# Kernel optimization log

Hardware: AMD Instinct MI355X
Metric: run time of the kernel (lower is better)

The kernel has to match this reference:

```python
import jax, jax.numpy as jnp
import numpy as np

KS = 3
STRIDE = 2
ALPHA = 16


def _parabolic_kernel(t, ks=KS, alpha=ALPHA):
    # z_i = linspace(-ks//2 + 1, ks//2, ks)  (python floor-div semantics)
    lo = (-ks) // 2 + 1
    hi = ks // 2
    z_i = jnp.linspace(float(lo), float(hi), ks, dtype=jnp.float32)
    z_c = z_i[:, None] ** 2 + z_i[None, :] ** 2            # [ks, ks]
    # per-channel structuring function h: [C, ks, ks]
    return -(z_c[None, :, :] / t[:, None, None]) ** alpha


def setup_inputs() -> dict:
    key = jax.random.key(0)
    kf, kt = jax.random.split(key)
    B, C, H, W = 16, 128, 224, 224
    f = jax.random.normal(kf, (B, C, H, W), dtype=jnp.float32)
    # init='uniform' -> U(0, 4); keep away from 0 to avoid fp32 overflow of (z/t)^16
    t = 0.5 + 3.5 * jax.random.uniform(kt, (C,), dtype=jnp.float32)
    return {"f": f, "t": t}


def reference(f, t):
    # Morphological dilation-style pooling: out = max over window of (f + h)
    h = _parabolic_kernel(t)                               # [C, ks, ks]
    B, C, H, W = f.shape
    Ho = (H - KS) // STRIDE + 1
    Wo = (W - KS) // STRIDE + 1
    out = jnp.full((B, C, Ho, Wo), -jnp.inf, dtype=f.dtype)
    for ki in range(KS):            # fixed 3x3 kernel: small static loop
        for kj in range(KS):
            win = f[:, :, ki:ki + (Ho - 1) * STRIDE + 1:STRIDE,
                          kj:kj + (Wo - 1) * STRIDE + 1:STRIDE]  # [B,C,Ho,Wo]
            out = jnp.maximum(out, win + h[None, :, ki, kj, None, None])
    return out
```

## Files before the change

### kernel.cpp

```cpp
#include <hip/hip_runtime.h>
#include <math.h>


namespace {
constexpr int Bn = 16, Cn = 128, Hn = 224, Wn = 224;
constexpr int Ho = 111, Wo = 111;
constexpr int ROWS_PER_BLOCK = 8;
}

__global__ __launch_bounds__(256) void lfp_kernel(const float* __restrict__ f,
                                                  const float* __restrict__ t,
                                                  float* __restrict__ out) {
    const int j  = threadIdx.x;
    const int bc = blockIdx.z;
    const int c  = bc & (Cn - 1);

    const float tc = t[c];
    const float xe = 1.0f / tc, xc = 2.0f / tc;
    float e2 = xe * xe, e4 = e2 * e2, e8 = e4 * e4;
    float c2 = xc * xc, c4 = c2 * c2, c8 = c4 * c4;
    const float hE = -(e8 * e8);
    const float hC = -(c8 * c8);

    if (j >= 56) return;
    const int col  = 4 * j;
    const int ecol = (col + 4 < Wn) ? col + 4 : Wn - 1;

    const float* fplane = f + (size_t)bc * Hn * Wn;
    float* oplane = out + (size_t)bc * Ho * Wo;

#pragma unroll
    for (int ii = 0; ii < 2; ++ii) {
        const int i = blockIdx.y * ROWS_PER_BLOCK + ii * 4 + threadIdx.y;
        if (i < Ho) {
            const float* base = fplane + (size_t)(2 * i) * Wn;
            float me = -INFINITY, mo = -INFINITY;
#pragma unroll
            for (int ki = 0; ki < 3; ++ki) {
                const float4 v = *(const float4*)(base + (size_t)ki * Wn + col);
                const float  e = base[(size_t)ki * Wn + ecol];
                const float hA = (ki == 1) ? hE : hC;
                const float hB = (ki == 1) ? 0.0f : hE;
                me = fmaxf(me, fmaxf(fmaxf(v.x + hA, v.y + hB), v.z + hA));
                mo = fmaxf(mo, fmaxf(fmaxf(v.z + hA, v.w + hB), e + hA));
            }
            float* orow = oplane + (size_t)i * Wo;
            orow[2 * j] = me;
            if (2 * j + 1 < Wo) orow[2 * j + 1] = mo;
        }
    }
}

extern "C" void kernel_launch(void* const* d_in, const int* in_sizes, int n_in,
                              void* d_out, int out_size, void* d_ws, size_t ws_size,
                              hipStream_t stream) {
    const float* f = (const float*)d_in[0];
    const float* t = (const float*)d_in[1];
    float* out = (float*)d_out;

    dim3 block(64, 4, 1);
    dim3 grid(1, (Ho + ROWS_PER_BLOCK - 1) / ROWS_PER_BLOCK, Bn * Cn);
    lfp_kernel<<<grid, block, 0, stream>>>(f, t, out);
}
```

Before: 560.1 us.

## Stream rows per thread with vertical reuse of shared boundary row and flat grid

Each thread now covers one column group and walks 37 consecutive output rows. The bottom input row of one output row is carried in registers and reused as the top row of the next, which cuts global loads per output from three rows to two. The 2D grid with idle lanes (56 of 64 active) becomes a dense 1D grid of exactly 3*planes*56 threads, and output writes use nontemporal stores. The trade-off is far fewer threads with a long serial loop per thread, which may lower memory-level parallelism and occupancy.

```diff
diff --git a/kernel.cpp b/kernel.cpp
--- a/kernel.cpp
+++ b/kernel.cpp
@@ -5,15 +5,20 @@
 namespace {
 constexpr int Bn = 16, Cn = 128, Hn = 224, Wn = 224;
 constexpr int Ho = 111, Wo = 111;
-constexpr int ROWS_PER_BLOCK = 8;
+constexpr int TILE = 37;
+constexpr int CT = 56;
+constexpr int PLANES = Bn * Cn;
 }
 
 __global__ __launch_bounds__(256) void lfp_kernel(const float* __restrict__ f,
                                                   const float* __restrict__ t,
                                                   float* __restrict__ out) {
-    const int j  = threadIdx.x;
-    const int bc = blockIdx.z;
-    const int c  = bc & (Cn - 1);
+    const int tid  = blockIdx.x * 256 + threadIdx.x;
+    const int flat = tid % (PLANES * CT);
+    const int rt   = tid / (PLANES * CT);
+    const int bc   = flat / CT;
+    const int jt   = flat % CT;
+    const int c    = bc & (Cn - 1);
 
     const float tc = t[c];
     const float xe = 1.0f / tc, xc = 2.0f / tc;
@@ -22,32 +27,45 @@
     const float hE = -(e8 * e8);
     const float hC = -(c8 * c8);
 
-    if (j >= 56) return;
-    const int col  = 4 * j;
+    const int col  = 4 * jt;
     const int ecol = (col + 4 < Wn) ? col + 4 : Wn - 1;
+    const bool oddValid = (2 * jt + 1) < Wo;
 
-    const float* fplane = f + (size_t)bc * Hn * Wn;
-    float* oplane = out + (size_t)bc * Ho * Wo;
+    const float* plane  = f + (size_t)bc * Hn * Wn;
+    float*       oplane = out + (size_t)bc * Ho * Wo;
 
-#pragma unroll
-    for (int ii = 0; ii < 2; ++ii) {
-        const int i = blockIdx.y * ROWS_PER_BLOCK + ii * 4 + threadIdx.y;
-        if (i < Ho) {
-            const float* base = fplane + (size_t)(2 * i) * Wn;
-            float me = -INFINITY, mo = -INFINITY;
-#pragma unroll
-            for (int ki = 0; ki < 3; ++ki) {
-                const float4 v = *(const float4*)(base + (size_t)ki * Wn + col);
-                const float  e = base[(size_t)ki * Wn + ecol];
-                const float hA = (ki == 1) ? hE : hC;
-                const float hB = (ki == 1) ? 0.0f : hE;
-                me = fmaxf(me, fmaxf(fmaxf(v.x + hA, v.y + hB), v.z + hA));
-                mo = fmaxf(mo, fmaxf(fmaxf(v.z + hA, v.w + hB), e + hA));
-            }
-            float* orow = oplane + (size_t)i * Wo;
-            orow[2 * j] = me;
-            if (2 * j + 1 < Wo) orow[2 * j + 1] = mo;
-        }
+    const int i0 = rt * TILE;
+
+    {
+    }
+    const float* r0 = plane + (size_t)(2 * i0) * Wn;
+    float4 v0 = *(const float4*)(r0 + col);
+    float  t0 = r0[ecol];
+    float prevOuterA = fmaxf(fmaxf(v0.x + hC, v0.y + hE), v0.z + hC);
+    float prevOuterB = fmaxf(fmaxf(v0.z + hC, v0.w + hE), t0 + hC);
+
+    for (int ii = 0; ii < TILE; ++ii) {
+        const int i = i0 + ii;
+        const float* rm = plane + (size_t)(2 * i + 1) * Wn;
+        const float* rb = plane + (size_t)(2 * i + 2) * Wn;
+        float4 vm = *(const float4*)(rm + col);
+        float  em = rm[ecol];
+        float4 vb = *(const float4*)(rb + col);
+        float  eb = rb[ecol];
+
+        float midA = fmaxf(fmaxf(vm.x + hE, vm.y), vm.z + hE);
+        float midB = fmaxf(fmaxf(vm.z + hE, vm.w), em + hE);
+        float outA = fmaxf(fmaxf(vb.x + hC, vb.y + hE), vb.z + hC);
+        float outB = fmaxf(fmaxf(vb.z + hC, vb.w + hE), eb + hC);
+
+        float oA = fmaxf(fmaxf(prevOuterA, midA), outA);
+        float oB = fmaxf(fmaxf(prevOuterB, midB), outB);
+        prevOuterA = outA;
+        prevOuterB = outB;
+
+        float* orow = oplane + (size_t)i * Wo + 2 * jt;
+        __builtin_nontemporal_store(oA, orow);
+        if (oddValid) __builtin_nontemporal_store(oB, orow + 1);
     }
 }
 
@@ -58,7 +76,7 @@
     const float* t = (const float*)d_in[1];
     float* out = (float*)d_out;
 
-    dim3 block(64, 4, 1);
-    dim3 grid(1, (Ho + ROWS_PER_BLOCK - 1) / ROWS_PER_BLOCK, Bn * Cn);
-    lfp_kernel<<<grid, block, 0, stream>>>(f, t, out);
+    const int total  = 3 * PLANES * CT;
+    const int blocks = total / 256;
+    lfp_kernel<<<dim3(blocks), dim3(256), 0, stream>>>(f, t, out);
 }
```

Result: slower. 666.8 us (+19.1%).
